# Kernel optimization log

Measured on AMD Instinct MI355X. Metric: run time of the kernel, lower is better.

The kernel has to match this reference:

```python
import jax, jax.numpy as jnp
import numpy as np

NQ, N, C = 8192, 32768, 128


def setup_inputs() -> dict:
    key = jax.random.key(0)
    k1, k2, k3 = jax.random.split(key, 3)
    return {
        "query_pos": jax.random.normal(k1, (NQ, 3), dtype=jnp.float32),
        "neural_feat": jax.random.normal(k2, (N, C), dtype=jnp.float32),
        "neural_pos": jax.random.normal(k3, (N, 3), dtype=jnp.float32),
        "knn": 64,
    }


def _cdist(a, b):
    # Euclidean pairwise distances via the (|a|^2 + |b|^2 - 2ab) expansion.
    a2 = jnp.sum(a * a, axis=-1, keepdims=True)          # [N',1]
    b2 = jnp.sum(b * b, axis=-1)                          # [N]
    d2 = a2 + b2[None, :] - 2.0 * (a @ b.T)               # [N',N]
    return jnp.sqrt(jnp.maximum(d2, 1e-12))


def reference(query_pos, neural_feat, neural_pos, knn):
    dists = _cdist(query_pos, neural_pos)                 # [N',N]
    # torch.topk(largest=False, sorted=True) == top_k of negated dists.
    neg_vals, closest_ind = jax.lax.top_k(-dists, knn)    # [N',k]
    closest_dists = -neg_vals                             # ascending
    closest_feat = neural_feat[closest_ind]               # [N',k,C] gather
    inv_dist = 1.0 / (closest_dists + 1e-5)               # [N',k]
    retrieved_feat = jnp.sum(closest_feat * inv_dist[..., None], axis=1)  # [N',C]
    return retrieved_feat
```

## Files before the change

kernel.cpp:

```cpp
#include <hip/hip_runtime.h>
#include <math.h>

#define NQ    8192
#define NPTS  32768
#define KNN   64
#define CAP   256
#define G     32
#define NCELLS (G*G*G)
#define GLO   (-4.8f)
#define GINV  (G / 9.6f)
#define NBLK  2048

__device__ __forceinline__ unsigned key_of(float f) {
  unsigned u = __float_as_uint(f);
  return (u & 0x80000000u) ? ~u : (u | 0x80000000u);
}
__device__ __forceinline__ float val_of(unsigned k) {
  unsigned u = (k & 0x80000000u) ? (k & 0x7fffffffu) : ~k;
  return __uint_as_float(u);
}
__device__ __forceinline__ int mbcnt64(unsigned long long m) {
  return __builtin_amdgcn_mbcnt_hi((unsigned)(m >> 32),
         __builtin_amdgcn_mbcnt_lo((unsigned)m, 0));
}
__device__ __forceinline__ float rflf(float x) {
  return __int_as_float(__builtin_amdgcn_readfirstlane(__float_as_int(x)));
}
__device__ __forceinline__ int rfli(int x) { return __builtin_amdgcn_readfirstlane(x); }

__device__ __forceinline__ float norm_cdf(float x) { return 0.5f * erfcf(-x * 0.70710678f); }
__device__ __forceinline__ float ball_mass(float mu, float r) {
  float a = r - mu, b = r + mu;
  float e = __expf(-0.5f * b * b) - __expf(-0.5f * a * a);
  return e / (mu * 2.50662827f) + norm_cdf(a) - norm_cdf(-mu) + norm_cdf(b) - norm_cdf(mu);
}

__device__ __forceinline__ int cidx(float v) {
  int i = (int)floorf((v - GLO) * GINV);
  return min(max(i, 0), G - 1);
}


__global__ __launch_bounds__(256) void hist_tau_kernel(
    const float* __restrict__ pos, const float* __restrict__ qpos,
    int* __restrict__ pcnt, int* __restrict__ qcnt, float* __restrict__ tau) {
  const int gid = blockIdx.x * 256 + threadIdx.x;
  const float x = pos[gid * 3 + 0], y = pos[gid * 3 + 1], z = pos[gid * 3 + 2];
  atomicAdd(&pcnt[(cidx(z) * G + cidx(y)) * G + cidx(x)], 1);
  if (gid < NQ) {
    const float qx = qpos[gid * 3 + 0], qy = qpos[gid * 3 + 1], qz = qpos[gid * 3 + 2];
    atomicAdd(&qcnt[(cidx(qz) * G + cidx(qy)) * G + cidx(qx)], 1);
    const float b = qx * qx + qy * qy + qz * qz;
    const float mu = fmaxf(sqrtf(b), 0.05f);
    const float target = 110.0f / 32768.0f;
    float lo = 0.f, hi = mu + 8.f;
    for (int i = 0; i < 16; ++i) {
      float r = 0.5f * (lo + hi);
      if (ball_mass(mu, r) < target) lo = r; else hi = r;
    }
    tau[gid] = hi * hi;
  }
}

__global__ __launch_bounds__(1024) void prefix_kernel(
    int* __restrict__ pcnt, int* __restrict__ start, int* __restrict__ qcnt) {
  __shared__ int sSum[1024];
  const int t = threadIdx.x;
  int* src = (blockIdx.x == 0) ? pcnt : qcnt;
  const int base = t * 32;
  int v[32];
  {
    const int4* cp = (const int4*)(src + base);
    #pragma unroll
    for (int j = 0; j < 8; ++j) { const int4 q = cp[j];
      v[j*4+0]=q.x; v[j*4+1]=q.y; v[j*4+2]=q.z; v[j*4+3]=q.w; }
  }
  int s = 0;
  #pragma unroll
  for (int j = 0; j < 32; ++j) { const int c = v[j]; v[j] = s; s += c; }
  sSum[t] = s;
  __syncthreads();
  for (int off = 1; off < 1024; off <<= 1) {
    const int u = (t >= off) ? sSum[t - off] : 0;
    __syncthreads();
    sSum[t] += u;
    __syncthreads();
  }
  const int excl = (t == 0) ? 0 : sSum[t - 1];
  if (blockIdx.x == 0) {
    #pragma unroll
    for (int j = 0; j < 8; ++j) {
      const int4 q = make_int4(excl+v[j*4], excl+v[j*4+1], excl+v[j*4+2], excl+v[j*4+3]);
      ((int4*)(start + base))[j] = q;
      ((int4*)(pcnt  + base))[j] = q;
    }
    if (t == 1023) start[NCELLS] = NPTS;
  } else {
    #pragma unroll
    for (int j = 0; j < 8; ++j) {
      const int4 q = make_int4(excl+v[j*4], excl+v[j*4+1], excl+v[j*4+2], excl+v[j*4+3]);
      ((int4*)(qcnt + base))[j] = q;
    }
  }
}

__global__ __launch_bounds__(256) void scatter_kernel(
    const float* __restrict__ pos, const float* __restrict__ qpos,
    int* __restrict__ pcur, int* __restrict__ qcur, const float* __restrict__ tau,
    float4* __restrict__ pts, float4* __restrict__ qp, float* __restrict__ qtau) {
  const int gid = blockIdx.x * 256 + threadIdx.x;
  const float x = pos[gid * 3 + 0], y = pos[gid * 3 + 1], z = pos[gid * 3 + 2];
  const int c = (cidx(z) * G + cidx(y)) * G + cidx(x);
  const int slot = atomicAdd(&pcur[c], 1);
  pts[slot] = make_float4(x, y, z, __int_as_float(gid));
  if (gid < NQ) {
    const float a = qpos[gid * 3 + 0], b = qpos[gid * 3 + 1], d = qpos[gid * 3 + 2];
    const int qc = (cidx(d) * G + cidx(b)) * G + cidx(a);
    const int qs = atomicAdd(&qcur[qc], 1);
    qp[qs] = make_float4(a, b, d, __int_as_float(gid));
    qtau[qs] = tau[gid];
  }
}


__global__ __launch_bounds__(256, 8) void knn_main(
    const float* __restrict__ feat, const int* __restrict__ cellStart,
    const float4* __restrict__ pts, const float4* __restrict__ qp,
    const float* __restrict__ qtau, float* __restrict__ out) {

  __shared__ uint2 sCand[4][CAP];
  __shared__ uint2 sSel[4][KNN];
  __shared__ int   sCum[4][64];
  __shared__ int   sAdj[4][64];

  const int tid = threadIdx.x, lane = tid & 63, wv = tid >> 6;
  const int bid = blockIdx.x;
  const int swz = (bid & 7) * (NBLK / 8) + (bid >> 3);
  const int sq  = swz * 4 + wv;

  const float4 Q = qp[sq];
  const float qx = rflf(Q.x), qy = rflf(Q.y), qz = rflf(Q.z);
  const int orig = rfli(__float_as_int(Q.w));
  const float bq = qx * qx + qy * qy + qz * qz;
  const float nx = -2.f * qx, ny = -2.f * qy, nz = -2.f * qz;
  float r2 = rflf(qtau[sq]);
  float tlo = 0.f, thi = -1.f;
  int cnt = 0;

  for (int attempt = 0; attempt < 12; ++attempt) {
    const float r = sqrtf(r2);
    const float tq = r2 - bq;
    const int ix0 = cidx(qx - r), ix1 = cidx(qx + r);
    const int iy0 = cidx(qy - r), iy1 = cidx(qy + r);
    const int iz0 = cidx(qz - r), iz1 = cidx(qz + r);
    const int nyw  = iy1 - iy0 + 1;
    const int nrow = nyw * (iz1 - iz0 + 1);
    cnt = 0;
    for (int rc = 0; rc < nrow; rc += 64) {
      const int myrow = rc + lane;
      int s = 0, c = 0;
      if (myrow < nrow) {
        const int dz = myrow / nyw;
        const int dy = myrow - dz * nyw;
        const int rb = ((iz0 + dz) * G + (iy0 + dy)) * G;
        s = cellStart[rb + ix0];
        c = cellStart[rb + ix1 + 1] - s;
      }
      int cum = c;
      #pragma unroll
      for (int off = 1; off < 64; off <<= 1) {
        const int u = __shfl_up(cum, off);
        if (lane >= off) cum += u;
      }
      sCum[wv][lane] = cum;
      sAdj[wv][lane] = s - (cum - c);
      const int Tc = __shfl(cum, 63);
      for (int b = 0; b < Tc; b += 64) {
        const int fi = b + lane;
        const bool have = fi < Tc;
        int ro = 0;
        #pragma unroll
        for (int st = 32; st; st >>= 1) {
          const int nr = ro + st;
          if (nr <= 64 && sCum[wv][nr - 1] <= fi) ro = nr;
        }
        const int pi = have ? fi + sAdj[wv][min(ro, 63)] : 0;
        const float4 P = pts[pi];
        const float n = P.x * P.x + P.y * P.y + P.z * P.z;
        const float d = fmaf(P.z, nz, fmaf(P.y, ny, fmaf(P.x, nx, n)));
        const bool h = have && (d < tq);
        const unsigned long long m = __ballot(h);
        if (m) {
          const int p = cnt + mbcnt64(m);
          if (h && p < CAP)
            sCand[wv][p] = make_uint2(key_of(d + bq), __float_as_uint(P.w));
          cnt += (int)__popcll(m);
        }
      }
    }
    if (cnt >= KNN && cnt <= CAP) break;
    if (cnt < KNN) { tlo = r2; r2 = (thi < 0.f) ? r2 * 3.f : 0.5f * (r2 + thi); }
    else           { thi = r2; r2 = 0.5f * (tlo + r2); }
  }

  {
    const int mm = min(cnt, CAP);
    unsigned k[4], id[4];
    #pragma unroll
    for (int s = 0; s < 4; ++s) {
      const int g2 = s * 64 + lane;
      uint2 kv = make_uint2(0xFFFFFFFFu, 0u);
      if (g2 < mm) kv = sCand[wv][g2];
      k[s] = kv.x; id[s] = kv.y;
    }
    unsigned blo = 0u, bhi = 0xFFFFFFFFu;
    for (int it = 0; it < 32; ++it) {
      const unsigned mid = blo + ((bhi - blo) >> 1);
      const int c = (int)(__popcll(__ballot(k[0] <= mid)) + __popcll(__ballot(k[1] <= mid)) +
                          __popcll(__ballot(k[2] <= mid)) + __popcll(__ballot(k[3] <= mid)));
      if (c >= KNN) bhi = mid; else blo = mid + 1;
    }
    const unsigned K = blo;

    int fill = 0;
    #pragma unroll
    for (int s = 0; s < 4; ++s) {
      const bool lt = k[s] < K;
      const unsigned long long msk = __ballot(lt);
      if (msk) {
        const int p = fill + mbcnt64(msk);
        if (lt) { const float dv = val_of(k[s]);
                  const float w_ = 1.f / (sqrtf(fmaxf(dv, 1e-12f)) + 1e-5f);
                  sSel[wv][p] = make_uint2(id[s], __float_as_uint(w_)); }
        fill += (int)__popcll(msk);
      }
    }
    #pragma unroll
    for (int s = 0; s < 4; ++s) {
      const bool eq = (k[s] == K);
      const unsigned long long msk = __ballot(eq);
      if (msk) {
        const int p = fill + mbcnt64(msk);
        if (eq && p < KNN) { const float dv = val_of(k[s]);
                             const float w_ = 1.f / (sqrtf(fmaxf(dv, 1e-12f)) + 1e-5f);
                             sSel[wv][p] = make_uint2(id[s], __float_as_uint(w_)); }
        fill += (int)__popcll(msk);
      }
    }
  }

  {
    float ax = 0.f, ay = 0.f;
    #pragma unroll 8
    for (int j = 0; j < KNN; ++j) {
      const uint2 pr = sSel[wv][j];
      const float w = __uint_as_float(pr.y);
      const float2 f2 = *(const float2*)(feat + ((size_t)pr.x << 7) + (lane << 1));
      ax = fmaf(w, f2.x, ax);
      ay = fmaf(w, f2.y, ay);
    }
    *(float2*)(out + ((size_t)orig << 7) + (lane << 1)) = make_float2(ax, ay);
  }
}

extern "C" void kernel_launch(void* const* d_in, const int* in_sizes, int n_in,
                              void* d_out, int out_size, void* d_ws, size_t ws_size,
                              hipStream_t stream) {
  const float* qpos = (const float*)d_in[0];
  const float* feat = (const float*)d_in[1];
  const float* pos  = (const float*)d_in[2];
  float* out = (float*)d_out;

  char* ws = (char*)d_ws;
  int*    pcnt      = (int*)(ws);
  int*    qcnt      = (int*)(ws + (128 << 10));
  int*    cellStart = (int*)(ws + (256 << 10));
  float*  tau       = (float*)(ws + (392 << 10));
  float4* pts       = (float4*)(ws + (424 << 10));
  float4* qp        = (float4*)(ws + (936 << 10));
  float*  qtau      = (float*)(ws + (1064 << 10));

  hipMemsetAsync(ws, 0, 256 << 10, stream);
  hist_tau_kernel<<<dim3(NPTS / 256), dim3(256),  0, stream>>>(pos, qpos, pcnt, qcnt, tau);
  prefix_kernel  <<<dim3(2),          dim3(1024), 0, stream>>>(pcnt, cellStart, qcnt);
  scatter_kernel <<<dim3(NPTS / 256), dim3(256),  0, stream>>>(pos, qpos, pcnt, qcnt, tau, pts, qp, qtau);
  knn_main       <<<dim3(NBLK),       dim3(256),  0, stream>>>(feat, cellStart, pts, qp, qtau, out);
}
```

Measured before the change: 134.0 us.

## Fuse grid build into one block, prune cell rows by sphere, widen gather

Replaces the memset plus three preprocessing kernels with a single 1024-thread block. That block builds the point and query cell grids in shared memory and estimates each query radius with a closed-form guess refined by two steps, replacing the 16-step bisection. The kNN kernel now handles rows in chunks of 16 and trims each row's x-range to the sphere's chord, finding the owning row with shuffles instead of shared arrays. The feature gather uses float4 loads split across two half-waves, followed by a shuffle reduction. The single-block preprocessing runs serially on one CU and may cost more than the launches it removes, and a looser radius guess can trigger more retry attempts.

```diff
diff --git a/kernel.cpp b/kernel.cpp
--- a/kernel.cpp
+++ b/kernel.cpp
@@ -8,8 +8,10 @@
 #define G     32
 #define NCELLS (G*G*G)
 #define GLO   (-4.8f)
+#define CELL  0.3f
 #define GINV  (G / 9.6f)
 #define NBLK  2048
+#define TGT   (110.0f / 32768.0f)
 
 __device__ __forceinline__ unsigned key_of(float f) {
   unsigned u = __float_as_uint(f);
@@ -41,84 +43,104 @@
 }
 
 
-__global__ __launch_bounds__(256) void hist_tau_kernel(
+__global__ __launch_bounds__(1024) void preproc_all(
     const float* __restrict__ pos, const float* __restrict__ qpos,
-    int* __restrict__ pcnt, int* __restrict__ qcnt, float* __restrict__ tau) {
-  const int gid = blockIdx.x * 256 + threadIdx.x;
-  const float x = pos[gid * 3 + 0], y = pos[gid * 3 + 1], z = pos[gid * 3 + 2];
-  atomicAdd(&pcnt[(cidx(z) * G + cidx(y)) * G + cidx(x)], 1);
-  if (gid < NQ) {
-    const float qx = qpos[gid * 3 + 0], qy = qpos[gid * 3 + 1], qz = qpos[gid * 3 + 2];
-    atomicAdd(&qcnt[(cidx(qz) * G + cidx(qy)) * G + cidx(qx)], 1);
-    const float b = qx * qx + qy * qy + qz * qz;
+    int* __restrict__ cellStart, float4* __restrict__ pts,
+    float4* __restrict__ qp, float* __restrict__ qtau) {
+
+  __shared__ int h[NCELLS];
+  __shared__ int aux[1024];
+  const int t = threadIdx.x;
+
+  #pragma unroll
+  for (int j = 0; j < NCELLS / 1024; ++j) h[t + 1024 * j] = 0;
+  __syncthreads();
+
+  int pc[32];
+  #pragma unroll
+  for (int j = 0; j < 32; ++j) {
+    const int i = t + 1024 * j;
+    const float x = pos[i * 3 + 0], y = pos[i * 3 + 1], z = pos[i * 3 + 2];
+    pc[j] = (cidx(z) * G + cidx(y)) * G + cidx(x);
+    atomicAdd(&h[pc[j]], 1);
+  }
+  __syncthreads();
+
+  {
+    const int base = t * 32;
+    int loc[32]; int s = 0;
+    #pragma unroll
+    for (int j = 0; j < 32; ++j) { loc[j] = s; s += h[base + j]; }
+    aux[t] = s; __syncthreads();
+    for (int off = 1; off < 1024; off <<= 1) {
+      const int v = (t >= off) ? aux[t - off] : 0; __syncthreads();
+      aux[t] += v; __syncthreads();
+    }
+    const int excl = t ? aux[t - 1] : 0;
+    #pragma unroll
+    for (int j = 0; j < 32; ++j) {
+      const int v = excl + loc[j];
+      cellStart[base + j] = v;
+      h[base + j] = v;
+    }
+    if (t == 1023) cellStart[NCELLS] = NPTS;
+  }
+  __syncthreads();
+
+  #pragma unroll
+  for (int j = 0; j < 32; ++j) {
+    const int i = t + 1024 * j;
+    const float x = pos[i * 3 + 0], y = pos[i * 3 + 1], z = pos[i * 3 + 2];
+    const int slot = atomicAdd(&h[pc[j]], 1);
+    pts[slot] = make_float4(x, y, z, __int_as_float(i));
+  }
+  __syncthreads();
+
+  #pragma unroll
+  for (int j = 0; j < NCELLS / 1024; ++j) h[t + 1024 * j] = 0;
+  __syncthreads();
+  int qc[8];
+  #pragma unroll
+  for (int j = 0; j < 8; ++j) {
+    const int i = t + 1024 * j;
+    const float x = qpos[i * 3 + 0], y = qpos[i * 3 + 1], z = qpos[i * 3 + 2];
+    qc[j] = (cidx(z) * G + cidx(y)) * G + cidx(x);
+    atomicAdd(&h[qc[j]], 1);
+  }
+  __syncthreads();
+  {
+    const int base = t * 32;
+    int loc[32]; int s = 0;
+    #pragma unroll
+    for (int j = 0; j < 32; ++j) { loc[j] = s; s += h[base + j]; }
+    aux[t] = s; __syncthreads();
+    for (int off = 1; off < 1024; off <<= 1) {
+      const int v = (t >= off) ? aux[t - off] : 0; __syncthreads();
+      aux[t] += v; __syncthreads();
+    }
+    const int excl = t ? aux[t - 1] : 0;
+    #pragma unroll
+    for (int j = 0; j < 32; ++j) h[base + j] = excl + loc[j];
+  }
+  __syncthreads();
+
+  #pragma unroll
+  for (int j = 0; j < 8; ++j) {
+    const int i = t + 1024 * j;
+    const float x = qpos[i * 3 + 0], y = qpos[i * 3 + 1], z = qpos[i * 3 + 2];
+    const float b = x * x + y * y + z * z;
     const float mu = fmaxf(sqrtf(b), 0.05f);
-    const float target = 110.0f / 32768.0f;
-    float lo = 0.f, hi = mu + 8.f;
-    for (int i = 0; i < 16; ++i) {
-      float r = 0.5f * (lo + hi);
-      if (ball_mass(mu, r) < target) lo = r; else hi = r;
-    }
-    tau[gid] = hi * hi;
-  }
-}
-
-__global__ __launch_bounds__(1024) void prefix_kernel(
-    int* __restrict__ pcnt, int* __restrict__ start, int* __restrict__ qcnt) {
-  __shared__ int sSum[1024];
-  const int t = threadIdx.x;
-  int* src = (blockIdx.x == 0) ? pcnt : qcnt;
-  const int base = t * 32;
-  int v[32];
-  {
-    const int4* cp = (const int4*)(src + base);
-    #pragma unroll
-    for (int j = 0; j < 8; ++j) { const int4 q = cp[j];
-      v[j*4+0]=q.x; v[j*4+1]=q.y; v[j*4+2]=q.z; v[j*4+3]=q.w; }
-  }
-  int s = 0;
-  #pragma unroll
-  for (int j = 0; j < 32; ++j) { const int c = v[j]; v[j] = s; s += c; }
-  sSum[t] = s;
-  __syncthreads();
-  for (int off = 1; off < 1024; off <<= 1) {
-    const int u = (t >= off) ? sSum[t - off] : 0;
-    __syncthreads();
-    sSum[t] += u;
-    __syncthreads();
-  }
-  const int excl = (t == 0) ? 0 : sSum[t - 1];
-  if (blockIdx.x == 0) {
-    #pragma unroll
-    for (int j = 0; j < 8; ++j) {
-      const int4 q = make_int4(excl+v[j*4], excl+v[j*4+1], excl+v[j*4+2], excl+v[j*4+3]);
-      ((int4*)(start + base))[j] = q;
-      ((int4*)(pcnt  + base))[j] = q;
-    }
-    if (t == 1023) start[NCELLS] = NPTS;
-  } else {
-    #pragma unroll
-    for (int j = 0; j < 8; ++j) {
-      const int4 q = make_int4(excl+v[j*4], excl+v[j*4+1], excl+v[j*4+2], excl+v[j*4+3]);
-      ((int4*)(qcnt + base))[j] = q;
-    }
-  }
-}
-
-__global__ __launch_bounds__(256) void scatter_kernel(
-    const float* __restrict__ pos, const float* __restrict__ qpos,
-    int* __restrict__ pcur, int* __restrict__ qcur, const float* __restrict__ tau,
-    float4* __restrict__ pts, float4* __restrict__ qp, float* __restrict__ qtau) {
-  const int gid = blockIdx.x * 256 + threadIdx.x;
-  const float x = pos[gid * 3 + 0], y = pos[gid * 3 + 1], z = pos[gid * 3 + 2];
-  const int c = (cidx(z) * G + cidx(y)) * G + cidx(x);
-  const int slot = atomicAdd(&pcur[c], 1);
-  pts[slot] = make_float4(x, y, z, __int_as_float(gid));
-  if (gid < NQ) {
-    const float a = qpos[gid * 3 + 0], b = qpos[gid * 3 + 1], d = qpos[gid * 3 + 2];
-    const int qc = (cidx(d) * G + cidx(b)) * G + cidx(a);
-    const int qs = atomicAdd(&qcur[qc], 1);
-    qp[qs] = make_float4(a, b, d, __int_as_float(gid));
-    qtau[qs] = tau[gid];
+    float r = 0.2329f * __expf(mu * mu * 0.16666667f);
+    r = fminf(r, mu + 6.0f);
+    #pragma unroll
+    for (int it = 0; it < 2; ++it) {
+      const float mss = fmaxf(ball_mass(mu, r), 1e-30f);
+      r = fminf(r * __powf(TGT / mss, 0.33333333f), mu + 6.0f);
+    }
+    r *= 1.10f;
+    const int slot = atomicAdd(&h[qc[j]], 1);
+    qp[slot] = make_float4(x, y, z, __int_as_float(i));
+    qtau[slot] = r * r;
   }
 }
 
@@ -130,8 +152,6 @@
 
   __shared__ uint2 sCand[4][CAP];
   __shared__ uint2 sSel[4][KNN];
-  __shared__ int   sCum[4][64];
-  __shared__ int   sAdj[4][64];
 
   const int tid = threadIdx.x, lane = tid & 63, wv = tid >> 6;
   const int bid = blockIdx.x;
@@ -150,49 +170,54 @@
   for (int attempt = 0; attempt < 12; ++attempt) {
     const float r = sqrtf(r2);
     const float tq = r2 - bq;
-    const int ix0 = cidx(qx - r), ix1 = cidx(qx + r);
     const int iy0 = cidx(qy - r), iy1 = cidx(qy + r);
     const int iz0 = cidx(qz - r), iz1 = cidx(qz + r);
     const int nyw  = iy1 - iy0 + 1;
     const int nrow = nyw * (iz1 - iz0 + 1);
     cnt = 0;
-    for (int rc = 0; rc < nrow; rc += 64) {
+    for (int rc = 0; rc < nrow; rc += 16) {
       const int myrow = rc + lane;
       int s = 0, c = 0;
-      if (myrow < nrow) {
+      if (lane < 16 && myrow < nrow) {
         const int dz = myrow / nyw;
         const int dy = myrow - dz * nyw;
-        const int rb = ((iz0 + dz) * G + (iy0 + dy)) * G;
-        s = cellStart[rb + ix0];
-        c = cellStart[rb + ix1 + 1] - s;
+        const int giy = iy0 + dy, giz = iz0 + dz;
+        const float ylo = GLO + giy * CELL;
+        const float zlo = GLO + giz * CELL;
+        const float dyv = fmaxf(0.f, fmaxf(ylo - qy, qy - (ylo + CELL)));
+        const float dzv = fmaxf(0.f, fmaxf(zlo - qz, qz - (zlo + CELL)));
+        const float dd = dyv * dyv + dzv * dzv;
+        if (dd < r2) {
+          const float hx = sqrtf(r2 - dd);
+          const int jx0 = cidx(qx - hx), jx1 = cidx(qx + hx);
+          const int rb = (giz * G + giy) * G;
+          s = cellStart[rb + jx0];
+          c = cellStart[rb + jx1 + 1] - s;
+        }
       }
       int cum = c;
       #pragma unroll
-      for (int off = 1; off < 64; off <<= 1) {
+      for (int off = 1; off < 16; off <<= 1) {
         const int u = __shfl_up(cum, off);
         if (lane >= off) cum += u;
       }
-      sCum[wv][lane] = cum;
-      sAdj[wv][lane] = s - (cum - c);
-      const int Tc = __shfl(cum, 63);
+      const int adj = s - (cum - c);
+      const int Tc = __shfl(cum, 15);
       for (int b = 0; b < Tc; b += 64) {
         const int fi = b + lane;
         const bool have = fi < Tc;
         int ro = 0;
         #pragma unroll
-        for (int st = 32; st; st >>= 1) {
-          const int nr = ro + st;
-          if (nr <= 64 && sCum[wv][nr - 1] <= fi) ro = nr;
-        }
-        const int pi = have ? fi + sAdj[wv][min(ro, 63)] : 0;
-        const float4 P = pts[pi];
+        for (int j = 0; j < 15; ++j) ro += (fi >= __shfl(cum, j));
+        const int pi = fi + __shfl(adj, ro);
+        const float4 P = pts[have ? pi : 0];
         const float n = P.x * P.x + P.y * P.y + P.z * P.z;
         const float d = fmaf(P.z, nz, fmaf(P.y, ny, fmaf(P.x, nx, n)));
-        const bool h = have && (d < tq);
-        const unsigned long long m = __ballot(h);
+        const bool hh = have && (d < tq);
+        const unsigned long long m = __ballot(hh);
         if (m) {
           const int p = cnt + mbcnt64(m);
-          if (h && p < CAP)
+          if (hh && p < CAP)
             sCand[wv][p] = make_uint2(key_of(d + bq), __float_as_uint(P.w));
           cnt += (int)__popcll(m);
         }
@@ -250,16 +275,25 @@
   }
 
   {
-    float ax = 0.f, ay = 0.f;
-    #pragma unroll 8
-    for (int j = 0; j < KNN; ++j) {
-      const uint2 pr = sSel[wv][j];
+    const int half = lane >> 5;
+    const int col  = lane & 31;
+    float4 acc = make_float4(0.f, 0.f, 0.f, 0.f);
+    #pragma unroll 4
+    for (int j = 0; j < KNN; j += 2) {
+      const uint2 pr = sSel[wv][j + half];
       const float w = __uint_as_float(pr.y);
-      const float2 f2 = *(const float2*)(feat + ((size_t)pr.x << 7) + (lane << 1));
-      ax = fmaf(w, f2.x, ax);
-      ay = fmaf(w, f2.y, ay);
-    }
-    *(float2*)(out + ((size_t)orig << 7) + (lane << 1)) = make_float2(ax, ay);
+      const float4 f4 = *(const float4*)(feat + ((size_t)pr.x << 7) + (col << 2));
+      acc.x = fmaf(w, f4.x, acc.x);
+      acc.y = fmaf(w, f4.y, acc.y);
+      acc.z = fmaf(w, f4.z, acc.z);
+      acc.w = fmaf(w, f4.w, acc.w);
+    }
+    acc.x += __shfl_xor(acc.x, 32);
+    acc.y += __shfl_xor(acc.y, 32);
+    acc.z += __shfl_xor(acc.z, 32);
+    acc.w += __shfl_xor(acc.w, 32);
+    if (lane < 32)
+      *(float4*)(out + ((size_t)orig << 7) + (col << 2)) = acc;
   }
 }
 
@@ -272,17 +306,11 @@
   float* out = (float*)d_out;
 
   char* ws = (char*)d_ws;
-  int*    pcnt      = (int*)(ws);
-  int*    qcnt      = (int*)(ws + (128 << 10));
-  int*    cellStart = (int*)(ws + (256 << 10));
-  float*  tau       = (float*)(ws + (392 << 10));
-  float4* pts       = (float4*)(ws + (424 << 10));
-  float4* qp        = (float4*)(ws + (936 << 10));
-  float*  qtau      = (float*)(ws + (1064 << 10));
-
-  hipMemsetAsync(ws, 0, 256 << 10, stream);
-  hist_tau_kernel<<<dim3(NPTS / 256), dim3(256),  0, stream>>>(pos, qpos, pcnt, qcnt, tau);
-  prefix_kernel  <<<dim3(2),          dim3(1024), 0, stream>>>(pcnt, cellStart, qcnt);
-  scatter_kernel <<<dim3(NPTS / 256), dim3(256),  0, stream>>>(pos, qpos, pcnt, qcnt, tau, pts, qp, qtau);
-  knn_main       <<<dim3(NBLK),       dim3(256),  0, stream>>>(feat, cellStart, pts, qp, qtau, out);
-}
+  int*    cellStart = (int*)(ws);
+  float4* pts       = (float4*)(ws + (132 << 10));
+  float4* qp        = (float4*)(ws + (644 << 10));
+  float*  qtau      = (float*)(ws + (772 << 10));
+
+  preproc_all<<<dim3(1),    dim3(1024), 0, stream>>>(pos, qpos, cellStart, pts, qp, qtau);
+  knn_main   <<<dim3(NBLK), dim3(256),  0, stream>>>(feat, cellStart, pts, qp, qtau, out);
+}
```

Result: slower. 451.6 us (+237.0%).

## Clip per-row x-range to sphere, compute tau in-kernel, widen feature gather

Applied to the files above, without the earlier changes.

Each row's x-extent of candidate cells is now clipped to the sphere's chord for that (y,z) row, so fewer points get scanned. Rows are processed 16 at a time, and the shared-memory cumulative arrays are replaced by shuffles. The tau bisection moves out of the histogram kernel into knn_main, which removes the tau and qtau buffers and their scatter. The final weighted gather now uses float4 loads, with two neighbours per wave handled in parallel and combined by an xor shuffle. The risks are redundant per-wave bisection work and less row parallelism in the scan loop.

```diff
diff --git a/kernel.cpp b/kernel.cpp
--- a/kernel.cpp
+++ b/kernel.cpp
@@ -8,8 +8,10 @@
 #define G     32
 #define NCELLS (G*G*G)
 #define GLO   (-4.8f)
+#define CELL  0.3f
 #define GINV  (G / 9.6f)
 #define NBLK  2048
+#define TGT   (110.0f / 32768.0f)
 
 __device__ __forceinline__ unsigned key_of(float f) {
   unsigned u = __float_as_uint(f);
@@ -41,24 +43,15 @@
 }
 
 
-__global__ __launch_bounds__(256) void hist_tau_kernel(
+__global__ __launch_bounds__(256) void hist_kernel(
     const float* __restrict__ pos, const float* __restrict__ qpos,
-    int* __restrict__ pcnt, int* __restrict__ qcnt, float* __restrict__ tau) {
+    int* __restrict__ pcnt, int* __restrict__ qcnt) {
   const int gid = blockIdx.x * 256 + threadIdx.x;
   const float x = pos[gid * 3 + 0], y = pos[gid * 3 + 1], z = pos[gid * 3 + 2];
   atomicAdd(&pcnt[(cidx(z) * G + cidx(y)) * G + cidx(x)], 1);
   if (gid < NQ) {
     const float qx = qpos[gid * 3 + 0], qy = qpos[gid * 3 + 1], qz = qpos[gid * 3 + 2];
     atomicAdd(&qcnt[(cidx(qz) * G + cidx(qy)) * G + cidx(qx)], 1);
-    const float b = qx * qx + qy * qy + qz * qz;
-    const float mu = fmaxf(sqrtf(b), 0.05f);
-    const float target = 110.0f / 32768.0f;
-    float lo = 0.f, hi = mu + 8.f;
-    for (int i = 0; i < 16; ++i) {
-      float r = 0.5f * (lo + hi);
-      if (ball_mass(mu, r) < target) lo = r; else hi = r;
-    }
-    tau[gid] = hi * hi;
   }
 }
 
@@ -106,8 +99,8 @@
 
 __global__ __launch_bounds__(256) void scatter_kernel(
     const float* __restrict__ pos, const float* __restrict__ qpos,
-    int* __restrict__ pcur, int* __restrict__ qcur, const float* __restrict__ tau,
-    float4* __restrict__ pts, float4* __restrict__ qp, float* __restrict__ qtau) {
+    int* __restrict__ pcur, int* __restrict__ qcur,
+    float4* __restrict__ pts, float4* __restrict__ qp) {
   const int gid = blockIdx.x * 256 + threadIdx.x;
   const float x = pos[gid * 3 + 0], y = pos[gid * 3 + 1], z = pos[gid * 3 + 2];
   const int c = (cidx(z) * G + cidx(y)) * G + cidx(x);
@@ -118,7 +111,6 @@
     const int qc = (cidx(d) * G + cidx(b)) * G + cidx(a);
     const int qs = atomicAdd(&qcur[qc], 1);
     qp[qs] = make_float4(a, b, d, __int_as_float(gid));
-    qtau[qs] = tau[gid];
   }
 }
 
@@ -126,12 +118,10 @@
 __global__ __launch_bounds__(256, 8) void knn_main(
     const float* __restrict__ feat, const int* __restrict__ cellStart,
     const float4* __restrict__ pts, const float4* __restrict__ qp,
-    const float* __restrict__ qtau, float* __restrict__ out) {
+    float* __restrict__ out) {
 
   __shared__ uint2 sCand[4][CAP];
   __shared__ uint2 sSel[4][KNN];
-  __shared__ int   sCum[4][64];
-  __shared__ int   sAdj[4][64];
 
   const int tid = threadIdx.x, lane = tid & 63, wv = tid >> 6;
   const int bid = blockIdx.x;
@@ -143,56 +133,71 @@
   const int orig = rfli(__float_as_int(Q.w));
   const float bq = qx * qx + qy * qy + qz * qz;
   const float nx = -2.f * qx, ny = -2.f * qy, nz = -2.f * qz;
-  float r2 = rflf(qtau[sq]);
+
+  float r2;
+  {
+    const float mu = fmaxf(sqrtf(bq), 0.05f);
+    float lo = 0.f, hi = mu + 8.f;
+    for (int i = 0; i < 16; ++i) {
+      const float rr = 0.5f * (lo + hi);
+      if (ball_mass(mu, rr) < TGT) lo = rr; else hi = rr;
+    }
+    r2 = hi * hi;
+  }
   float tlo = 0.f, thi = -1.f;
   int cnt = 0;
 
   for (int attempt = 0; attempt < 12; ++attempt) {
     const float r = sqrtf(r2);
     const float tq = r2 - bq;
-    const int ix0 = cidx(qx - r), ix1 = cidx(qx + r);
     const int iy0 = cidx(qy - r), iy1 = cidx(qy + r);
     const int iz0 = cidx(qz - r), iz1 = cidx(qz + r);
     const int nyw  = iy1 - iy0 + 1;
     const int nrow = nyw * (iz1 - iz0 + 1);
     cnt = 0;
-    for (int rc = 0; rc < nrow; rc += 64) {
+    for (int rc = 0; rc < nrow; rc += 16) {
       const int myrow = rc + lane;
       int s = 0, c = 0;
-      if (myrow < nrow) {
+      if (lane < 16 && myrow < nrow) {
         const int dz = myrow / nyw;
         const int dy = myrow - dz * nyw;
-        const int rb = ((iz0 + dz) * G + (iy0 + dy)) * G;
-        s = cellStart[rb + ix0];
-        c = cellStart[rb + ix1 + 1] - s;
+        const int giy = iy0 + dy, giz = iz0 + dz;
+        const float ylo = GLO + giy * CELL;
+        const float zlo = GLO + giz * CELL;
+        const float dyv = fmaxf(0.f, fmaxf(ylo - qy, qy - (ylo + CELL)));
+        const float dzv = fmaxf(0.f, fmaxf(zlo - qz, qz - (zlo + CELL)));
+        const float dd = dyv * dyv + dzv * dzv;
+        if (dd < r2) {
+          const float hx = sqrtf(r2 - dd);
+          const int jx0 = cidx(qx - hx), jx1 = cidx(qx + hx);
+          const int rb = (giz * G + giy) * G;
+          s = cellStart[rb + jx0];
+          c = cellStart[rb + jx1 + 1] - s;
+        }
       }
       int cum = c;
       #pragma unroll
-      for (int off = 1; off < 64; off <<= 1) {
+      for (int off = 1; off < 16; off <<= 1) {
         const int u = __shfl_up(cum, off);
         if (lane >= off) cum += u;
       }
-      sCum[wv][lane] = cum;
-      sAdj[wv][lane] = s - (cum - c);
-      const int Tc = __shfl(cum, 63);
+      const int adj = s - (cum - c);
+      const int Tc = __shfl(cum, 15);
       for (int b = 0; b < Tc; b += 64) {
         const int fi = b + lane;
         const bool have = fi < Tc;
         int ro = 0;
         #pragma unroll
-        for (int st = 32; st; st >>= 1) {
-          const int nr = ro + st;
-          if (nr <= 64 && sCum[wv][nr - 1] <= fi) ro = nr;
-        }
-        const int pi = have ? fi + sAdj[wv][min(ro, 63)] : 0;
-        const float4 P = pts[pi];
+        for (int j = 0; j < 15; ++j) ro += (fi >= __shfl(cum, j));
+        const int pi = fi + __shfl(adj, ro);
+        const float4 P = pts[have ? pi : 0];
         const float n = P.x * P.x + P.y * P.y + P.z * P.z;
         const float d = fmaf(P.z, nz, fmaf(P.y, ny, fmaf(P.x, nx, n)));
-        const bool h = have && (d < tq);
-        const unsigned long long m = __ballot(h);
+        const bool hh = have && (d < tq);
+        const unsigned long long m = __ballot(hh);
         if (m) {
           const int p = cnt + mbcnt64(m);
-          if (h && p < CAP)
+          if (hh && p < CAP)
             sCand[wv][p] = make_uint2(key_of(d + bq), __float_as_uint(P.w));
           cnt += (int)__popcll(m);
         }
@@ -250,16 +255,25 @@
   }
 
   {
-    float ax = 0.f, ay = 0.f;
-    #pragma unroll 8
-    for (int j = 0; j < KNN; ++j) {
-      const uint2 pr = sSel[wv][j];
+    const int half = lane >> 5;
+    const int col  = lane & 31;
+    float4 acc = make_float4(0.f, 0.f, 0.f, 0.f);
+    #pragma unroll 4
+    for (int j = 0; j < KNN; j += 2) {
+      const uint2 pr = sSel[wv][j + half];
       const float w = __uint_as_float(pr.y);
-      const float2 f2 = *(const float2*)(feat + ((size_t)pr.x << 7) + (lane << 1));
-      ax = fmaf(w, f2.x, ax);
-      ay = fmaf(w, f2.y, ay);
-    }
-    *(float2*)(out + ((size_t)orig << 7) + (lane << 1)) = make_float2(ax, ay);
+      const float4 f4 = *(const float4*)(feat + ((size_t)pr.x << 7) + (col << 2));
+      acc.x = fmaf(w, f4.x, acc.x);
+      acc.y = fmaf(w, f4.y, acc.y);
+      acc.z = fmaf(w, f4.z, acc.z);
+      acc.w = fmaf(w, f4.w, acc.w);
+    }
+    acc.x += __shfl_xor(acc.x, 32);
+    acc.y += __shfl_xor(acc.y, 32);
+    acc.z += __shfl_xor(acc.z, 32);
+    acc.w += __shfl_xor(acc.w, 32);
+    if (lane < 32)
+      *(float4*)(out + ((size_t)orig << 7) + (col << 2)) = acc;
   }
 }
 
@@ -275,14 +289,12 @@
   int*    pcnt      = (int*)(ws);
   int*    qcnt      = (int*)(ws + (128 << 10));
   int*    cellStart = (int*)(ws + (256 << 10));
-  float*  tau       = (float*)(ws + (392 << 10));
-  float4* pts       = (float4*)(ws + (424 << 10));
-  float4* qp        = (float4*)(ws + (936 << 10));
-  float*  qtau      = (float*)(ws + (1064 << 10));
+  float4* pts       = (float4*)(ws + (392 << 10));
+  float4* qp        = (float4*)(ws + (904 << 10));
 
   hipMemsetAsync(ws, 0, 256 << 10, stream);
-  hist_tau_kernel<<<dim3(NPTS / 256), dim3(256),  0, stream>>>(pos, qpos, pcnt, qcnt, tau);
-  prefix_kernel  <<<dim3(2),          dim3(1024), 0, stream>>>(pcnt, cellStart, qcnt);
-  scatter_kernel <<<dim3(NPTS / 256), dim3(256),  0, stream>>>(pos, qpos, pcnt, qcnt, tau, pts, qp, qtau);
-  knn_main       <<<dim3(NBLK),       dim3(256),  0, stream>>>(feat, cellStart, pts, qp, qtau, out);
-}
+  hist_kernel   <<<dim3(NPTS / 256), dim3(256),  0, stream>>>(pos, qpos, pcnt, qcnt);
+  prefix_kernel <<<dim3(2),          dim3(1024), 0, stream>>>(pcnt, cellStart, qcnt);
+  scatter_kernel<<<dim3(NPTS / 256), dim3(256),  0, stream>>>(pos, qpos, pcnt, qcnt, pts, qp);
+  knn_main      <<<dim3(NBLK),       dim3(256),  0, stream>>>(feat, cellStart, pts, qp, out);
+}
```

New measurement: 147.8 us. +10.3%, slower.
